# Kernel tuning notes

Measured on AMD Instinct MI355X. Metric: run time of the kernel, lower is better.

The kernel has to match this reference:

```python
import jax, jax.numpy as jnp
import numpy as np

# Model dims (match init_kwargs): dim=768, num_heads=12, num_kv_heads=2 -> G=6, head_dim=64
DIM, HKV, G, D = 768, 2, 6, 64


def setup_inputs() -> dict:
    key = jax.random.key(0)
    ks = jax.random.split(key, 9)
    w = 0.02  # init scale for weights
    return {
        "x": jax.random.normal(ks[0], (8, 1024, DIM), dtype=jnp.float32),
        "depth_k": jax.random.normal(ks[1], (8, 1024, HKV, D), dtype=jnp.float32),
        "depth_v": jax.random.normal(ks[2], (8, 1024, HKV, D), dtype=jnp.float32),
        "Wq": jax.random.normal(ks[3], (DIM, DIM), dtype=jnp.float32) * w,
        "bq": jnp.zeros((DIM,), dtype=jnp.float32),
        "Wkv": jax.random.normal(ks[4], (2 * HKV * D, DIM), dtype=jnp.float32) * w,
        "bkv": jnp.zeros((2 * HKV * D,), dtype=jnp.float32),
        "Wproj": jax.random.normal(ks[5], (DIM, DIM), dtype=jnp.float32) * w,
        "bproj": jnp.zeros((DIM,), dtype=jnp.float32),
    }


def reference(x, depth_k, depth_v, Wq, bq, Wkv, bkv, Wproj, bproj):
    B, N, C = x.shape
    scale = D ** -0.5
    # Q projection, GQA groups unfolded into the sequence dim: [B, N*G, Hkv, D]
    q = (x @ Wq.T + bq).reshape(B, N * G, HKV, D)
    # KV projection: [B, N, 2, Hkv, D]
    kv = (x @ Wkv.T + bkv).reshape(B, N, 2, HKV, D)
    k, v = kv[:, :, 0], kv[:, :, 1]
    # Concatenate depth (previous-layer) KV cache along the sequence dim
    k_full = jnp.concatenate([depth_k, k], axis=1)  # [B, N_cache+N, Hkv, D]
    v_full = jnp.concatenate([depth_v, v], axis=1)
    # Full (non-causal) attention per kv head over the unfolded query sequence
    scores = jnp.einsum('bqhd,bkhd->bhqk', q, k_full) * scale  # [B, Hkv, N*G, Kv]
    attn = jax.nn.softmax(scores, axis=-1)
    o = jnp.einsum('bhqk,bkhd->bqhd', attn, v_full)  # [B, N*G, Hkv, D]
    out = o.reshape(B, N, C) @ Wproj.T + bproj  # fold G*Hkv*D back to C=dim
    return out, k, v
```

## Files before the change

kernel.cpp:

```cpp
#include <hip/hip_runtime.h>

using sh8 = __attribute__((ext_vector_type(8))) short;
using sh4 = __attribute__((ext_vector_type(4))) short;
using fx4 = __attribute__((ext_vector_type(4))) float;

#define MFMA(a,b,c)   __builtin_amdgcn_mfma_f32_16x16x32_bf16((a),(b),(c),0,0,0)

__device__ __forceinline__ short f2bf(float f) {
    union { float f; unsigned u; } v; v.f = f;
    return (short)((v.u + 0x7fffu + ((v.u >> 16) & 1u)) >> 16);
}

__device__ __forceinline__ unsigned cvtpk(float lo, float hi) {
    unsigned r;
    asm("v_cvt_pk_bf16_f32 %0, %1, %2" : "=v"(r) : "v"(lo), "v"(hi));
    return r;
}

__device__ __forceinline__ sh8 pack8(float4 a, float4 b) {
    union { unsigned u[4]; sh8 s; } r;
    r.u[0] = cvtpk(a.x, a.y);
    r.u[1] = cvtpk(a.z, a.w);
    r.u[2] = cvtpk(b.x, b.y);
    r.u[3] = cvtpk(b.z, b.w);
    return r.s;
}

#define QSCALE 0.18033688011112042f

#define GLOAD_LDS16(gsrc, ldst) __builtin_amdgcn_global_load_lds( \
    (const __attribute__((address_space(1))) void*)(gsrc),        \
    (__attribute__((address_space(3))) void*)(ldst), 16, 0, 0)

__global__ __launch_bounds__(256) void cast_k(const float* __restrict__ x,
                                              const float* __restrict__ Wq,
                                              const float* __restrict__ Wkv,
                                              short* __restrict__ xbf,
                                              short* __restrict__ wqbf,
                                              short* __restrict__ wkvbf)
{
    const int blk = blockIdx.x, t = threadIdx.x;
    const float* src; short* dst; size_t idx8;
    if (blk < 3072)      { src = x;   dst = xbf;   idx8 = ((size_t)blk * 256 + t) * 8; }
    else if (blk < 3360) { src = Wq;  dst = wqbf;  idx8 = ((size_t)(blk - 3072) * 256 + t) * 8; }
    else                 { src = Wkv; dst = wkvbf; idx8 = ((size_t)(blk - 3360) * 256 + t) * 8; }
    float4 a = *(const float4*)(src + idx8);
    float4 b = *(const float4*)(src + idx8 + 4);
    *(sh8*)&dst[idx8] = pack8(a, b);
}


__global__ __launch_bounds__(256) void prep_k(const short* __restrict__ xbf,
                                              const short* __restrict__ wqbf,
                                              const short* __restrict__ wkvbf,
                                              const float* __restrict__ bq,
                                              const float* __restrict__ bkv,
                                              const float* __restrict__ dk,
                                              const float* __restrict__ dv,
                                              float* __restrict__ ok,
                                              float* __restrict__ ov,
                                              short* __restrict__ q_ws,
                                              short* __restrict__ k_ws,
                                              short* __restrict__ vT_ws)
{
    __shared__ alignas(16) short Al[128 * 40];
    __shared__ alignas(16) short Bl[128 * 40];
    const int blk = blockIdx.x;
    const int t   = threadIdx.x;

    if (blk < 512) {
        const int x8 = blk & 7, jj = blk >> 3;
        const int m  = x8 * 8 + (jj >> 3);
        const int nn = jj & 7;
        const bool isq = (nn < 6);
        const int  bm  = m * 128, bn = (isq ? nn : nn - 6) * 128;
        const short* Wmat = isq ? wqbf : wkvbf;

        const int wave = t >> 6, lane = t & 63;
        const int wm   = wave >> 1, wn = wave & 1;
        const int lhi  = lane >> 4, llo = lane & 15;

        const int srow = t >> 1, scol = (t & 1) * 16;
        const short* ap = xbf  + (size_t)(bm + srow) * 768 + scol;
        const short* bp = Wmat + (size_t)(bn + srow) * 768 + scol;

        fx4 zero = {0.f, 0.f, 0.f, 0.f};
        fx4 acc[4][4];
        #pragma unroll
        for (int a = 0; a < 4; ++a)
            #pragma unroll
            for (int b2 = 0; b2 < 4; ++b2) acc[a][b2] = zero;

        sh8 qa0 = *(const sh8*)(ap), qa1 = *(const sh8*)(ap + 8);
        sh8 qb0 = *(const sh8*)(bp), qb1 = *(const sh8*)(bp + 8);

        for (int k0 = 0; k0 < 768; k0 += 32) {
            __syncthreads();
            *(sh8*)&Al[srow*40 + scol]     = qa0;
            *(sh8*)&Al[srow*40 + scol + 8] = qa1;
            *(sh8*)&Bl[srow*40 + scol]     = qb0;
            *(sh8*)&Bl[srow*40 + scol + 8] = qb1;
            __syncthreads();
            if (k0 + 32 < 768) {
                qa0 = *(const sh8*)(ap + k0+32);  qa1 = *(const sh8*)(ap + k0+40);
                qb0 = *(const sh8*)(bp + k0+32);  qb1 = *(const sh8*)(bp + k0+40);
            }
            sh8 af[4], bf[4];
            #pragma unroll
            for (int mt = 0; mt < 4; ++mt)
                af[mt] = *(const sh8*)&Al[(wm*64 + mt*16 + llo)*40 + lhi*8];
            #pragma unroll
            for (int nt = 0; nt < 4; ++nt)
                bf[nt] = *(const sh8*)&Bl[(wn*64 + nt*16 + llo)*40 + lhi*8];
            #pragma unroll
            for (int mt = 0; mt < 4; ++mt)
                #pragma unroll
                for (int nt = 0; nt < 4; ++nt)
                    acc[mt][nt] = MFMA(af[mt], bf[nt], acc[mt][nt]);
        }

        if (isq) {
            #pragma unroll
            for (int nt = 0; nt < 4; ++nt) {
                const int c = bn + wn*64 + nt*16 + llo;
                const float bias = bq[c];
                const int g = c >> 7, h = (c >> 6) & 1, d = c & 63;
                #pragma unroll
                for (int mt = 0; mt < 4; ++mt) {
                    const int m0 = bm + wm*64 + mt*16 + lhi*4;
                    #pragma unroll
                    for (int r = 0; r < 4; ++r) {
                        const int mr = m0 + r;
                        const int b = mr >> 10, n = mr & 1023;
                        const float val = (acc[mt][nt][r] + bias) * QSCALE;
                        q_ws[((size_t)(b*2 + h)*6144 + n*6 + g)*64 + d] = f2bf(val);
                    }
                }
            }
        } else {
            #pragma unroll
            for (int nt = 0; nt < 4; ++nt) {
                const int c = bn + wn*64 + nt*16 + llo;
                const float bias = bkv[c];
                const int s = c >> 7, h = (c >> 6) & 1, d = c & 63;
                #pragma unroll
                for (int mt = 0; mt < 4; ++mt) {
                    const int m0 = bm + wm*64 + mt*16 + lhi*4;
                    const int b = m0 >> 10, n0 = m0 & 1023;
                    float vals[4];
                    #pragma unroll
                    for (int r = 0; r < 4; ++r) vals[r] = acc[mt][nt][r] + bias;
                    const int key = 1024 + n0;
                    if (s == 0) {
                        #pragma unroll
                        for (int r = 0; r < 4; ++r)
                            ok[((size_t)(b*1024 + n0 + r)*2 + h)*64 + d] = vals[r];
                        const int kb_ = key >> 6, nt_ = (key >> 4) & 3;
                        const int half = d >> 5, lhiK = (d >> 3) & 3, jK = d & 7;
                        const size_t base = (size_t)(b*2 + h)*131072
                            + (size_t)(((((kb_*4 + nt_)*2 + half)*64) + lhiK*16 + (key & 15))*8 + jK);
                        #pragma unroll
                        for (int r = 0; r < 4; ++r)
                            k_ws[base + r*8] = f2bf(vals[r]);
                    } else {
                        #pragma unroll
                        for (int r = 0; r < 4; ++r)
                            ov[((size_t)(b*1024 + n0 + r)*2 + h)*64 + d] = vals[r];
                        const int kb_ = key >> 6, g_ = (key >> 5) & 1, k5 = key & 31;
                        const int half5 = k5 >> 4, lhi5 = (k5 >> 2) & 3;
                        const int dt_ = d >> 4, llov = d & 15;
                        short4 pk = make_short4(f2bf(vals[0]), f2bf(vals[1]),
                                                f2bf(vals[2]), f2bf(vals[3]));
                        const size_t base = (size_t)(b*2 + h)*131072
                            + (size_t)(((((kb_*2 + g_)*4 + dt_)*64) + lhi5*16 + llov)*8 + half5*4);
                        *(short4*)&vT_ws[base] = pk;
                    }
                }
            }
        }
    } else if (blk < 1536) {
        const size_t idx4 = ((size_t)(blk - 512) * 256 + t) * 4;
        const int b  = (int)(idx4 >> 17);
        const int rm = (int)(idx4 & 131071);
        const int tt = rm >> 7, h = (rm >> 6) & 1, d = rm & 63;
        float4 v = *(const float4*)(dk + idx4);
        short4 pk = make_short4(f2bf(v.x), f2bf(v.y), f2bf(v.z), f2bf(v.w));
        const int kb_ = tt >> 6, nt_ = (tt >> 4) & 3, lloK = tt & 15;
        const int half = d >> 5, lhiK = (d >> 3) & 3, jK = d & 7;
        const size_t addr = (size_t)(b*2 + h)*131072
            + (size_t)(((((kb_*4 + nt_)*2 + half)*64) + lhiK*16 + lloK)*8 + jK);
        *(short4*)&k_ws[addr] = pk;
    } else {
        const int unit = (blk - 1536)*4 + (t >> 6);
        const int lane = t & 63, lhi = lane >> 4, llo = lane & 15;
        const int dt_ = unit & 3, g_ = (unit >> 2) & 1;
        const int kb_ = (unit >> 3) & 15, bh = unit >> 7;
        const int b = bh >> 1, h = bh & 1;
        const float* s0 = dv
            + ((size_t)((b*1024 + kb_*64 + g_*32 + lhi*4)*2 + h))*64 + dt_*16 + llo;
        union { short s[8]; sh8 v8; } o;
        #pragma unroll
        for (int jv = 0; jv < 4; ++jv) o.s[jv]     = f2bf(s0[(size_t)jv * 128]);
        #pragma unroll
        for (int jv = 0; jv < 4; ++jv) o.s[4 + jv] = f2bf(s0[(size_t)(16 + jv) * 128]);
        *(sh8*)&vT_ws[((size_t)bh*256 + (kb_*2 + g_)*4 + dt_)*512 + lane*8] = o.v8;
    }
}

__global__ __launch_bounds__(256) void attn_k(const short* __restrict__ q_ws,
                                              const short* __restrict__ k_ws,
                                              const short* __restrict__ vT_ws,
                                              short* __restrict__ o_ws)
{
    __shared__ alignas(16) short L[4][8][512];
    const int t    = threadIdx.x;
    const int wave = t >> 6, lane = t & 63;
    const int lhi  = lane >> 4, llo = lane & 15;
    const int blk  = blockIdx.x;
    const int x8   = blk & 7, jj = blk >> 3;
    const int bh   = x8 * 2 + (jj >= 48 ? 1 : 0);
    const int qt   = (jj >= 48) ? (jj - 48) : jj;
    const int b    = bh >> 1, h = bh & 1;

    const short* qb = q_ws + ((size_t)bh*6144 + qt*128 + wave*32) * 64;
    sh8 qf[2][2];
    #pragma unroll
    for (int s = 0; s < 2; ++s) {
        qf[s][0] = *(const sh8*)(qb + (s*16 + llo)*64 + lhi*8);
        qf[s][1] = *(const sh8*)(qb + (s*16 + llo)*64 + lhi*8 + 32);
    }

    const short* kbase = k_ws  + (size_t)bh*131072;
    const short* vbase = vT_ws + (size_t)bh*131072;

    fx4 zero = {0.f, 0.f, 0.f, 0.f};
    fx4 oacc[2][4];
    fx4 lacc[2];
    #pragma unroll
    for (int s = 0; s < 2; ++s) {
        lacc[s] = zero;
        #pragma unroll
        for (int dt = 0; dt < 4; ++dt) oacc[s][dt] = zero;
    }

    union { unsigned u[4]; sh8 s8; } onesu;
    onesu.u[0] = onesu.u[1] = onesu.u[2] = onesu.u[3] = 0x3F803F80u;
    const sh8 ones = onesu.s8;

    auto stage = [&](int g) {
        const short* ks = kbase + ((size_t)g*4 + wave)*512 + lane*8;
        const short* vs = vbase + ((size_t)g*4 + wave)*512 + lane*8;
        GLOAD_LDS16(ks, &L[g & 3][wave][0]);
        GLOAD_LDS16(vs, &L[g & 3][4 + wave][0]);
    };

    stage(0);
    stage(1);

    for (int g = 0; g < 64; ++g) {
        if (g < 62) {
            stage(g + 2);
            asm volatile("s_waitcnt vmcnt(4)" ::: "memory");
        } else if (g == 62) {
            asm volatile("s_waitcnt vmcnt(2)" ::: "memory");
        } else {
            asm volatile("s_waitcnt vmcnt(0)" ::: "memory");
        }
        __builtin_amdgcn_s_barrier();
        __builtin_amdgcn_sched_barrier(0);

        const short* Lb = (const short*)&L[g & 3][0][0];
        const int lo = lane * 8;
        sh8 K0 = *(const sh8*)(Lb + lo);
        sh8 K1 = *(const sh8*)(Lb + 512  + lo);
        sh8 K2 = *(const sh8*)(Lb + 1024 + lo);
        sh8 K3 = *(const sh8*)(Lb + 1536 + lo);
        sh8 V0 = *(const sh8*)(Lb + 2048 + lo);
        sh8 V1 = *(const sh8*)(Lb + 2560 + lo);
        sh8 V2 = *(const sh8*)(Lb + 3072 + lo);
        sh8 V3 = *(const sh8*)(Lb + 3584 + lo);

        #pragma unroll
        for (int s = 0; s < 2; ++s) {
            fx4 stA = MFMA(K0, qf[s][0], zero); stA = MFMA(K1, qf[s][1], stA);
            fx4 stB = MFMA(K2, qf[s][0], zero); stB = MFMA(K3, qf[s][1], stB);
            float pa0 = __builtin_amdgcn_exp2f(stA[0]);
            float pa1 = __builtin_amdgcn_exp2f(stA[1]);
            float pa2 = __builtin_amdgcn_exp2f(stA[2]);
            float pa3 = __builtin_amdgcn_exp2f(stA[3]);
            float pb0 = __builtin_amdgcn_exp2f(stB[0]);
            float pb1 = __builtin_amdgcn_exp2f(stB[1]);
            float pb2 = __builtin_amdgcn_exp2f(stB[2]);
            float pb3 = __builtin_amdgcn_exp2f(stB[3]);
            union { unsigned u[4]; sh8 s8; } pu;
            pu.u[0] = cvtpk(pa0, pa1);
            pu.u[1] = cvtpk(pa2, pa3);
            pu.u[2] = cvtpk(pb0, pb1);
            pu.u[3] = cvtpk(pb2, pb3);
            lacc[s]    = MFMA(pu.s8, ones, lacc[s]);
            oacc[s][0] = MFMA(pu.s8, V0, oacc[s][0]);
            oacc[s][1] = MFMA(pu.s8, V1, oacc[s][1]);
            oacc[s][2] = MFMA(pu.s8, V2, oacc[s][2]);
            oacc[s][3] = MFMA(pu.s8, V3, oacc[s][3]);
        }
    }

    #pragma unroll
    for (int s = 0; s < 2; ++s) {
        #pragma unroll
        for (int r = 0; r < 4; ++r) {
            const float iq = 1.0f / lacc[s][r];
            const int qi = qt*128 + wave*32 + s*16 + lhi*4 + r;
            const int n = qi / 6, g = qi % 6;
            short* orow = o_ws + ((size_t)(b*1024 + n))*768 + g*128 + h*64;
            #pragma unroll
            for (int dt = 0; dt < 4; ++dt)
                orow[dt*16 + llo] = f2bf(oacc[s][dt][r] * iq);
        }
    }
}

__global__ __launch_bounds__(256) void projgemm_k(const short* __restrict__ o_ws,
                                                  const float* __restrict__ Wp,
                                                  const float* __restrict__ bpj,
                                                  float* __restrict__ out)
{
    __shared__ alignas(16) short Al[128 * 40];
    __shared__ alignas(16) short Bl[64 * 40];
    const int t    = threadIdx.x;
    const int wave = t >> 6, lane = t & 63;
    const int wm   = wave >> 1, wn = wave & 1;
    const int lhi  = lane >> 4, llo = lane & 15;
    const int x8   = blockIdx.x & 7, jj = blockIdx.x >> 3;
    const int bm   = (x8*8 + jj/12) * 128;
    const int bn   = (jj % 12) * 64;

    const int srow = t >> 1, scol = (t & 1) * 16;
    const int brow = t >> 2, bcol = (t & 3) * 8;
    const short* ap = o_ws + (size_t)(bm + srow) * 768 + scol;
    const float* bp = Wp   + (size_t)(bn + brow) * 768 + bcol;

    fx4 zero = {0.f, 0.f, 0.f, 0.f};
    fx4 acc[4][2];
    #pragma unroll
    for (int i = 0; i < 4; ++i)
        #pragma unroll
        for (int j2 = 0; j2 < 2; ++j2) acc[i][j2] = zero;

    sh8 qa0 = *(const sh8*)(ap), qa1 = *(const sh8*)(ap + 8);
    float4 pb0 = *(const float4*)(bp), pb1 = *(const float4*)(bp + 4);

    for (int k0 = 0; k0 < 768; k0 += 32) {
        __syncthreads();
        *(sh8*)&Al[srow*40 + scol] = qa0;
        *(sh8*)&Al[srow*40 + scol + 8] = qa1;
        *(sh8*)&Bl[brow*40 + bcol] = pack8(pb0, pb1);
        __syncthreads();
        if (k0 + 32 < 768) {
            qa0 = *(const sh8*)(ap + k0+32);  qa1 = *(const sh8*)(ap + k0+40);
            pb0 = *(const float4*)(bp + k0+32);  pb1 = *(const float4*)(bp + k0+36);
        }
        sh8 af[4], bf[2];
        #pragma unroll
        for (int mt = 0; mt < 4; ++mt)
            af[mt] = *(const sh8*)&Al[(wm*64 + mt*16 + llo)*40 + lhi*8];
        #pragma unroll
        for (int nt = 0; nt < 2; ++nt)
            bf[nt] = *(const sh8*)&Bl[(wn*32 + nt*16 + llo)*40 + lhi*8];
        #pragma unroll
        for (int mt = 0; mt < 4; ++mt)
            #pragma unroll
            for (int nt = 0; nt < 2; ++nt)
                acc[mt][nt] = MFMA(af[mt], bf[nt], acc[mt][nt]);
    }

    #pragma unroll
    for (int nt = 0; nt < 2; ++nt) {
        const int c = bn + wn*32 + nt*16 + llo;
        const float bias = bpj[c];
        #pragma unroll
        for (int mt = 0; mt < 4; ++mt) {
            const int m0 = bm + wm*64 + mt*16 + lhi*4;
            #pragma unroll
            for (int r = 0; r < 4; ++r)
                out[(size_t)(m0 + r)*768 + c] = acc[mt][nt][r] + bias;
        }
    }
}

extern "C" void kernel_launch(void* const* d_in, const int* in_sizes, int n_in,
                              void* d_out, int out_size, void* d_ws, size_t ws_size,
                              hipStream_t stream)
{
    const float* x   = (const float*)d_in[0];
    const float* dk  = (const float*)d_in[1];
    const float* dv  = (const float*)d_in[2];
    const float* Wq  = (const float*)d_in[3];
    const float* bq  = (const float*)d_in[4];
    const float* Wkv = (const float*)d_in[5];
    const float* bkv = (const float*)d_in[6];
    const float* Wp  = (const float*)d_in[7];
    const float* bpj = (const float*)d_in[8];

    float* out = (float*)d_out;
    float* ok  = out + 6291456;
    float* ov  = out + 7340032;

    short* xbf   = (short*)out;
    short* wqbf  = xbf + 6291456;
    short* wkvbf = wqbf + 589824;

    char* ws = (char*)d_ws;
    short* q_ws  = (short*)(ws);
    short* k_ws  = (short*)(ws + 12582912);
    short* vT_ws = (short*)(ws + 16777216);
    short* o_ws  = (short*)(ws + 20971520);

    cast_k     <<<dim3(3456), 256, 0, stream>>>(x, Wq, Wkv, xbf, wqbf, wkvbf);
    prep_k     <<<dim3(2048), 256, 0, stream>>>(xbf, wqbf, wkvbf, bq, bkv, dk, dv,
                                                ok, ov, q_ws, k_ws, vT_ws);
    attn_k     <<<dim3(768),  256, 0, stream>>>(q_ws, k_ws, vT_ws, o_ws);
    projgemm_k <<<dim3(768),  256, 0, stream>>>(o_ws, Wp, bpj, out);
}
```

Measured before the change: 211.4 us.

## Split attention work across 8 waves with 16 query rows each

The attention kernel moves from 4 waves handling 32 query rows each to 8 waves handling 16 rows each. Each wave now issues a single async K or V tile load per stage. The MFMA against a ones vector for the row sum is replaced by a scalar fp32 sum of the exponentials, followed by cross-lane shuffles. The aim is more waves in flight to hide latency and fewer MFMAs, at the cost of reading the K/V shared tile from twice as many waves and extra shuffle work at the end.

```diff
diff --git a/kernel.cpp b/kernel.cpp
--- a/kernel.cpp
+++ b/kernel.cpp
@@ -207,10 +207,10 @@
     }
 }
 
-__global__ __launch_bounds__(256) void attn_k(const short* __restrict__ q_ws,
-                                              const short* __restrict__ k_ws,
-                                              const short* __restrict__ vT_ws,
-                                              short* __restrict__ o_ws)
+__global__ __launch_bounds__(512, 6) void attn_k(const short* __restrict__ q_ws,
+                                                 const short* __restrict__ k_ws,
+                                                 const short* __restrict__ vT_ws,
+                                                 short* __restrict__ o_ws)
 {
     __shared__ alignas(16) short L[4][8][512];
     const int t    = threadIdx.x;
@@ -222,37 +222,21 @@
     const int qt   = (jj >= 48) ? (jj - 48) : jj;
     const int b    = bh >> 1, h = bh & 1;
 
-    const short* qb = q_ws + ((size_t)bh*6144 + qt*128 + wave*32) * 64;
-    sh8 qf[2][2];
+    const short* qb = q_ws + ((size_t)bh*6144 + qt*128 + wave*16) * 64;
+    sh8 qf0 = *(const sh8*)(qb + llo*64 + lhi*8);
+    sh8 qf1 = *(const sh8*)(qb + llo*64 + lhi*8 + 32);
+
+    const short* cbase = (wave < 4 ? k_ws : vT_ws) + (size_t)bh*131072
+                         + (size_t)(wave & 3)*512 + lane*8;
+    auto stage = [&](int g) {
+        GLOAD_LDS16(cbase + (size_t)g*2048, &L[g & 3][wave][0]);
+    };
+
+    fx4 zero = {0.f, 0.f, 0.f, 0.f};
+    fx4 oacc[4];
     #pragma unroll
-    for (int s = 0; s < 2; ++s) {
-        qf[s][0] = *(const sh8*)(qb + (s*16 + llo)*64 + lhi*8);
-        qf[s][1] = *(const sh8*)(qb + (s*16 + llo)*64 + lhi*8 + 32);
-    }
-
-    const short* kbase = k_ws  + (size_t)bh*131072;
-    const short* vbase = vT_ws + (size_t)bh*131072;
-
-    fx4 zero = {0.f, 0.f, 0.f, 0.f};
-    fx4 oacc[2][4];
-    fx4 lacc[2];
-    #pragma unroll
-    for (int s = 0; s < 2; ++s) {
-        lacc[s] = zero;
-        #pragma unroll
-        for (int dt = 0; dt < 4; ++dt) oacc[s][dt] = zero;
-    }
-
-    union { unsigned u[4]; sh8 s8; } onesu;
-    onesu.u[0] = onesu.u[1] = onesu.u[2] = onesu.u[3] = 0x3F803F80u;
-    const sh8 ones = onesu.s8;
-
-    auto stage = [&](int g) {
-        const short* ks = kbase + ((size_t)g*4 + wave)*512 + lane*8;
-        const short* vs = vbase + ((size_t)g*4 + wave)*512 + lane*8;
-        GLOAD_LDS16(ks, &L[g & 3][wave][0]);
-        GLOAD_LDS16(vs, &L[g & 3][4 + wave][0]);
-    };
+    for (int dt = 0; dt < 4; ++dt) oacc[dt] = zero;
+    float lsum = 0.f;
 
     stage(0);
     stage(1);
@@ -260,9 +244,9 @@
     for (int g = 0; g < 64; ++g) {
         if (g < 62) {
             stage(g + 2);
-            asm volatile("s_waitcnt vmcnt(4)" ::: "memory");
+            asm volatile("s_waitcnt vmcnt(2)" ::: "memory");
         } else if (g == 62) {
-            asm volatile("s_waitcnt vmcnt(2)" ::: "memory");
+            asm volatile("s_waitcnt vmcnt(1)" ::: "memory");
         } else {
             asm volatile("s_waitcnt vmcnt(0)" ::: "memory");
         }
@@ -280,43 +264,41 @@
         sh8 V2 = *(const sh8*)(Lb + 3072 + lo);
         sh8 V3 = *(const sh8*)(Lb + 3584 + lo);
 
-        #pragma unroll
-        for (int s = 0; s < 2; ++s) {
-            fx4 stA = MFMA(K0, qf[s][0], zero); stA = MFMA(K1, qf[s][1], stA);
-            fx4 stB = MFMA(K2, qf[s][0], zero); stB = MFMA(K3, qf[s][1], stB);
-            float pa0 = __builtin_amdgcn_exp2f(stA[0]);
-            float pa1 = __builtin_amdgcn_exp2f(stA[1]);
-            float pa2 = __builtin_amdgcn_exp2f(stA[2]);
-            float pa3 = __builtin_amdgcn_exp2f(stA[3]);
-            float pb0 = __builtin_amdgcn_exp2f(stB[0]);
-            float pb1 = __builtin_amdgcn_exp2f(stB[1]);
-            float pb2 = __builtin_amdgcn_exp2f(stB[2]);
-            float pb3 = __builtin_amdgcn_exp2f(stB[3]);
-            union { unsigned u[4]; sh8 s8; } pu;
-            pu.u[0] = cvtpk(pa0, pa1);
-            pu.u[1] = cvtpk(pa2, pa3);
-            pu.u[2] = cvtpk(pb0, pb1);
-            pu.u[3] = cvtpk(pb2, pb3);
-            lacc[s]    = MFMA(pu.s8, ones, lacc[s]);
-            oacc[s][0] = MFMA(pu.s8, V0, oacc[s][0]);
-            oacc[s][1] = MFMA(pu.s8, V1, oacc[s][1]);
-            oacc[s][2] = MFMA(pu.s8, V2, oacc[s][2]);
-            oacc[s][3] = MFMA(pu.s8, V3, oacc[s][3]);
-        }
+        fx4 stA = MFMA(K0, qf0, zero); stA = MFMA(K1, qf1, stA);
+        fx4 stB = MFMA(K2, qf0, zero); stB = MFMA(K3, qf1, stB);
+        float pa0 = __builtin_amdgcn_exp2f(stA[0]);
+        float pa1 = __builtin_amdgcn_exp2f(stA[1]);
+        float pa2 = __builtin_amdgcn_exp2f(stA[2]);
+        float pa3 = __builtin_amdgcn_exp2f(stA[3]);
+        float pb0 = __builtin_amdgcn_exp2f(stB[0]);
+        float pb1 = __builtin_amdgcn_exp2f(stB[1]);
+        float pb2 = __builtin_amdgcn_exp2f(stB[2]);
+        float pb3 = __builtin_amdgcn_exp2f(stB[3]);
+        lsum += ((pa0 + pa1) + (pa2 + pa3)) + ((pb0 + pb1) + (pb2 + pb3));
+        union { unsigned u[4]; sh8 s8; } pu;
+        pu.u[0] = cvtpk(pa0, pa1);
+        pu.u[1] = cvtpk(pa2, pa3);
+        pu.u[2] = cvtpk(pb0, pb1);
+        pu.u[3] = cvtpk(pb2, pb3);
+        oacc[0] = MFMA(pu.s8, V0, oacc[0]);
+        oacc[1] = MFMA(pu.s8, V1, oacc[1]);
+        oacc[2] = MFMA(pu.s8, V2, oacc[2]);
+        oacc[3] = MFMA(pu.s8, V3, oacc[3]);
     }
 
+    lsum += __shfl_xor(lsum, 16, 64);
+    lsum += __shfl_xor(lsum, 32, 64);
+    const float inv = 1.0f / lsum;
+
     #pragma unroll
-    for (int s = 0; s < 2; ++s) {
-        #pragma unroll
-        for (int r = 0; r < 4; ++r) {
-            const float iq = 1.0f / lacc[s][r];
-            const int qi = qt*128 + wave*32 + s*16 + lhi*4 + r;
-            const int n = qi / 6, g = qi % 6;
-            short* orow = o_ws + ((size_t)(b*1024 + n))*768 + g*128 + h*64;
-            #pragma unroll
-            for (int dt = 0; dt < 4; ++dt)
-                orow[dt*16 + llo] = f2bf(oacc[s][dt][r] * iq);
-        }
+    for (int r = 0; r < 4; ++r) {
+        const float iq = __shfl(inv, lhi*4 + r, 64);
+        const int qi = qt*128 + wave*16 + lhi*4 + r;
+        const int n = qi / 6, g6 = qi % 6;
+        short* orow = o_ws + ((size_t)(b*1024 + n))*768 + g6*128 + h*64;
+        #pragma unroll
+        for (int dt = 0; dt < 4; ++dt)
+            orow[dt*16 + llo] = f2bf(oacc[dt][r] * iq);
     }
 }
 
@@ -419,6 +401,6 @@
     cast_k     <<<dim3(3456), 256, 0, stream>>>(x, Wq, Wkv, xbf, wqbf, wkvbf);
     prep_k     <<<dim3(2048), 256, 0, stream>>>(xbf, wqbf, wkvbf, bq, bkv, dk, dv,
                                                 ok, ov, q_ws, k_ws, vT_ws);
-    attn_k     <<<dim3(768),  256, 0, stream>>>(q_ws, k_ws, vT_ws, o_ws);
+    attn_k     <<<dim3(768),  512, 0, stream>>>(q_ws, k_ws, vT_ws, o_ws);
     projgemm_k <<<dim3(768),  256, 0, stream>>>(o_ws, Wp, bpj, out);
 }
```

Measured after the change: 220.1 us. 1.04x slower.

## Pipeline GEMM tiles with direct global-to-LDS loads and pre-cast Wproj to bf16

Applied to the files above, without the earlier changes.

Both the QKV projection GEMM and the output projection GEMM now stage tiles with asynchronous global-to-LDS 16-byte loads into a 4-slot ring buffer, prefetching two stages ahead. Explicit vmcnt waits and a single barrier per step replace the register-staged double sync. LDS is laid out in MFMA fragment order so each lane reads its fragment contiguously. A new kernel converts Wproj to bf16 into the now-unused q workspace before the projection GEMM, so the GEMM no longer converts fp32 per tile, at the cost of one extra launch.

```diff
diff --git a/kernel.cpp b/kernel.cpp
--- a/kernel.cpp
+++ b/kernel.cpp
@@ -47,6 +47,15 @@
     float4 a = *(const float4*)(src + idx8);
     float4 b = *(const float4*)(src + idx8 + 4);
     *(sh8*)&dst[idx8] = pack8(a, b);
+}
+
+__global__ __launch_bounds__(256) void wpcast_k(const float* __restrict__ Wp,
+                                                short* __restrict__ wpbf)
+{
+    const size_t idx8 = ((size_t)blockIdx.x * 256 + threadIdx.x) * 8;
+    float4 a = *(const float4*)(Wp + idx8);
+    float4 b = *(const float4*)(Wp + idx8 + 4);
+    *(sh8*)&wpbf[idx8] = pack8(a, b);
 }
 
 
@@ -63,8 +72,7 @@
                                               short* __restrict__ k_ws,
                                               short* __restrict__ vT_ws)
 {
-    __shared__ alignas(16) short Al[128 * 40];
-    __shared__ alignas(16) short Bl[128 * 40];
+    __shared__ alignas(16) short L[4][16][512];
     const int blk = blockIdx.x;
     const int t   = threadIdx.x;
 
@@ -79,10 +87,20 @@
         const int wave = t >> 6, lane = t & 63;
         const int wm   = wave >> 1, wn = wave & 1;
         const int lhi  = lane >> 4, llo = lane & 15;
-
-        const int srow = t >> 1, scol = (t & 1) * 16;
-        const short* ap = xbf  + (size_t)(bm + srow) * 768 + scol;
-        const short* bp = Wmat + (size_t)(bn + srow) * 768 + scol;
+        const int l15  = lane & 15, l4 = lane >> 4;
+
+        const short* aSrc0 = xbf  + (size_t)(bm + wave*16     + l15)*768 + l4*8;
+        const short* aSrc1 = xbf  + (size_t)(bm + (wave+4)*16 + l15)*768 + l4*8;
+        const short* bSrc0 = Wmat + (size_t)(bn + wave*16     + l15)*768 + l4*8;
+        const short* bSrc1 = Wmat + (size_t)(bn + (wave+4)*16 + l15)*768 + l4*8;
+
+        auto stage = [&](int s) {
+            const int r = s & 3;
+            GLOAD_LDS16(aSrc0 + s*32, &L[r][wave][0]);
+            GLOAD_LDS16(aSrc1 + s*32, &L[r][4 + wave][0]);
+            GLOAD_LDS16(bSrc0 + s*32, &L[r][8 + wave][0]);
+            GLOAD_LDS16(bSrc1 + s*32, &L[r][12 + wave][0]);
+        };
 
         fx4 zero = {0.f, 0.f, 0.f, 0.f};
         fx4 acc[4][4];
@@ -91,27 +109,30 @@
             #pragma unroll
             for (int b2 = 0; b2 < 4; ++b2) acc[a][b2] = zero;
 
-        sh8 qa0 = *(const sh8*)(ap), qa1 = *(const sh8*)(ap + 8);
-        sh8 qb0 = *(const sh8*)(bp), qb1 = *(const sh8*)(bp + 8);
-
-        for (int k0 = 0; k0 < 768; k0 += 32) {
-            __syncthreads();
-            *(sh8*)&Al[srow*40 + scol]     = qa0;
-            *(sh8*)&Al[srow*40 + scol + 8] = qa1;
-            *(sh8*)&Bl[srow*40 + scol]     = qb0;
-            *(sh8*)&Bl[srow*40 + scol + 8] = qb1;
-            __syncthreads();
-            if (k0 + 32 < 768) {
-                qa0 = *(const sh8*)(ap + k0+32);  qa1 = *(const sh8*)(ap + k0+40);
-                qb0 = *(const sh8*)(bp + k0+32);  qb1 = *(const sh8*)(bp + k0+40);
+        stage(0);
+        stage(1);
+
+        for (int s = 0; s < 24; ++s) {
+            if (s < 22) {
+                stage(s + 2);
+                asm volatile("s_waitcnt vmcnt(8)" ::: "memory");
+            } else if (s == 22) {
+                asm volatile("s_waitcnt vmcnt(4)" ::: "memory");
+            } else {
+                asm volatile("s_waitcnt vmcnt(0)" ::: "memory");
             }
+            __builtin_amdgcn_s_barrier();
+            __builtin_amdgcn_sched_barrier(0);
+
+            const short* Lb = (const short*)&L[s & 3][0][0];
+            const int lo = lane * 8;
             sh8 af[4], bf[4];
             #pragma unroll
             for (int mt = 0; mt < 4; ++mt)
-                af[mt] = *(const sh8*)&Al[(wm*64 + mt*16 + llo)*40 + lhi*8];
+                af[mt] = *(const sh8*)(Lb + (wm*4 + mt)*512 + lo);
             #pragma unroll
             for (int nt = 0; nt < 4; ++nt)
-                bf[nt] = *(const sh8*)&Bl[(wn*64 + nt*16 + llo)*40 + lhi*8];
+                bf[nt] = *(const sh8*)(Lb + (8 + wn*4 + nt)*512 + lo);
             #pragma unroll
             for (int mt = 0; mt < 4; ++mt)
                 #pragma unroll
@@ -321,24 +342,30 @@
 }
 
 __global__ __launch_bounds__(256) void projgemm_k(const short* __restrict__ o_ws,
-                                                  const float* __restrict__ Wp,
+                                                  const short* __restrict__ wpbf,
                                                   const float* __restrict__ bpj,
                                                   float* __restrict__ out)
 {
-    __shared__ alignas(16) short Al[128 * 40];
-    __shared__ alignas(16) short Bl[64 * 40];
+    __shared__ alignas(16) short L[4][12][512];
     const int t    = threadIdx.x;
     const int wave = t >> 6, lane = t & 63;
     const int wm   = wave >> 1, wn = wave & 1;
     const int lhi  = lane >> 4, llo = lane & 15;
+    const int l15  = lane & 15, l4 = lane >> 4;
     const int x8   = blockIdx.x & 7, jj = blockIdx.x >> 3;
     const int bm   = (x8*8 + jj/12) * 128;
     const int bn   = (jj % 12) * 64;
 
-    const int srow = t >> 1, scol = (t & 1) * 16;
-    const int brow = t >> 2, bcol = (t & 3) * 8;
-    const short* ap = o_ws + (size_t)(bm + srow) * 768 + scol;
-    const float* bp = Wp   + (size_t)(bn + brow) * 768 + bcol;
+    const short* aSrc0 = o_ws + (size_t)(bm + wave*16     + l15)*768 + l4*8;
+    const short* aSrc1 = o_ws + (size_t)(bm + (wave+4)*16 + l15)*768 + l4*8;
+    const short* bSrc  = wpbf + (size_t)(bn + wave*16     + l15)*768 + l4*8;
+
+    auto stage = [&](int s) {
+        const int r = s & 3;
+        GLOAD_LDS16(aSrc0 + s*32, &L[r][wave][0]);
+        GLOAD_LDS16(aSrc1 + s*32, &L[r][4 + wave][0]);
+        GLOAD_LDS16(bSrc  + s*32, &L[r][8 + wave][0]);
+    };
 
     fx4 zero = {0.f, 0.f, 0.f, 0.f};
     fx4 acc[4][2];
@@ -347,26 +374,30 @@
         #pragma unroll
         for (int j2 = 0; j2 < 2; ++j2) acc[i][j2] = zero;
 
-    sh8 qa0 = *(const sh8*)(ap), qa1 = *(const sh8*)(ap + 8);
-    float4 pb0 = *(const float4*)(bp), pb1 = *(const float4*)(bp + 4);
-
-    for (int k0 = 0; k0 < 768; k0 += 32) {
-        __syncthreads();
-        *(sh8*)&Al[srow*40 + scol] = qa0;
-        *(sh8*)&Al[srow*40 + scol + 8] = qa1;
-        *(sh8*)&Bl[brow*40 + bcol] = pack8(pb0, pb1);
-        __syncthreads();
-        if (k0 + 32 < 768) {
-            qa0 = *(const sh8*)(ap + k0+32);  qa1 = *(const sh8*)(ap + k0+40);
-            pb0 = *(const float4*)(bp + k0+32);  pb1 = *(const float4*)(bp + k0+36);
-        }
+    stage(0);
+    stage(1);
+
+    for (int s = 0; s < 24; ++s) {
+        if (s < 22) {
+            stage(s + 2);
+            asm volatile("s_waitcnt vmcnt(6)" ::: "memory");
+        } else if (s == 22) {
+            asm volatile("s_waitcnt vmcnt(3)" ::: "memory");
+        } else {
+            asm volatile("s_waitcnt vmcnt(0)" ::: "memory");
+        }
+        __builtin_amdgcn_s_barrier();
+        __builtin_amdgcn_sched_barrier(0);
+
+        const short* Lb = (const short*)&L[s & 3][0][0];
+        const int lo = lane * 8;
         sh8 af[4], bf[2];
         #pragma unroll
         for (int mt = 0; mt < 4; ++mt)
-            af[mt] = *(const sh8*)&Al[(wm*64 + mt*16 + llo)*40 + lhi*8];
+            af[mt] = *(const sh8*)(Lb + (wm*4 + mt)*512 + lo);
         #pragma unroll
         for (int nt = 0; nt < 2; ++nt)
-            bf[nt] = *(const sh8*)&Bl[(wn*32 + nt*16 + llo)*40 + lhi*8];
+            bf[nt] = *(const sh8*)(Lb + (8 + wn*2 + nt)*512 + lo);
         #pragma unroll
         for (int mt = 0; mt < 4; ++mt)
             #pragma unroll
@@ -416,9 +447,12 @@
     short* vT_ws = (short*)(ws + 16777216);
     short* o_ws  = (short*)(ws + 20971520);
 
+    short* wpbf  = q_ws;
+
     cast_k     <<<dim3(3456), 256, 0, stream>>>(x, Wq, Wkv, xbf, wqbf, wkvbf);
     prep_k     <<<dim3(2048), 256, 0, stream>>>(xbf, wqbf, wkvbf, bq, bkv, dk, dv,
                                                 ok, ov, q_ws, k_ws, vT_ws);
     attn_k     <<<dim3(768),  256, 0, stream>>>(q_ws, k_ws, vT_ws, o_ws);
-    projgemm_k <<<dim3(768),  256, 0, stream>>>(o_ws, Wp, bpj, out);
-}
+    wpcast_k   <<<dim3(288),  256, 0, stream>>>(Wp, wpbf);
+    projgemm_k <<<dim3(768),  256, 0, stream>>>(o_ws, wpbf, bpj, out);
+}
```

After: 209.2 us (median of 2 runs). About the same (-1.0%).
